# Kernel tuning notes

Measured on AMD Instinct MI355X. Metric: run time of the kernel, lower is better.

Reference implementation:

```python
import jax, jax.numpy as jnp
import numpy as np

B, L, H, NH, F = 32, 200, 256, 4, 2
D = H // NH
C = (2 + F) ** 2  # 16 fused attention streams (queries x keys)
SCALE = np.float32(1.0 / np.sqrt(D))
EPS = 1e-12


def setup_inputs() -> dict:
    key = jax.random.key(0)
    ks = jax.random.split(key, 16)
    p = lambda k, sh: jax.random.normal(k, sh, jnp.float32) * 0.02
    causal = jnp.tril(jnp.ones((L, L), jnp.float32))
    return {
        "input_tensor": jax.random.normal(ks[0], (B, L, H), jnp.float32),
        "attribute_table": jax.random.normal(ks[1], (F, B, L, 1, H), jnp.float32),
        "position_embedding": jax.random.normal(ks[2], (B, L, H), jnp.float32),
        "attention_mask": ((1.0 - causal) * -10000.0)[None, None],  # [1,1,L,L] additive causal mask
        "Wq": p(ks[3], (H, H)), "bq": jnp.zeros((H,), jnp.float32),
        "Wk": p(ks[4], (H, H)), "bk": jnp.zeros((H,), jnp.float32),
        "Wv": p(ks[5], (H, H)), "bv": jnp.zeros((H,), jnp.float32),
        "Wqp": p(ks[6], (H, H)), "bqp": jnp.zeros((H,), jnp.float32),
        "Wkp": p(ks[7], (H, H)), "bkp": jnp.zeros((H,), jnp.float32),
        "Wvp": p(ks[8], (H, H)), "bvp": jnp.zeros((H,), jnp.float32),
        "Wq_a": p(ks[9], (F, H, H)), "bq_a": jnp.zeros((F, H), jnp.float32),
        "Wk_a": p(ks[10], (F, H, H)), "bk_a": jnp.zeros((F, H), jnp.float32),
        "Wv_a": p(ks[11], (F, H, H)), "bv_a": jnp.zeros((F, H), jnp.float32),
        "Wf1": p(ks[12], (L, L)), "bf1": jnp.zeros((L,), jnp.float32),
        "Wf2": p(ks[13], (L, 1)), "bf2": jnp.zeros((1,), jnp.float32),
        "Wd": p(ks[14], (H, H)), "bd": jnp.zeros((H,), jnp.float32),
        "gamma": jnp.ones((H,), jnp.float32),
        "beta": jnp.zeros((H,), jnp.float32),
    }


def _forward(input_tensor, attribute_table, position_embedding, attention_mask,
             Wq, bq, Wk, bk, Wv, bv, Wqp, bqp, Wkp, bkp, Wvp, bvp,
             Wq_a, bq_a, Wk_a, bk_a, Wv_a, bv_a,
             Wf1, bf1, Wf2, bf2, Wd, bd, gamma, beta):
    Bv = input_tensor.shape[0]
    heads = lambda x: x.reshape(Bv, L, NH, D).transpose(0, 2, 1, 3)  # [B,h,L,d]
    q_i = heads(input_tensor @ Wq + bq)
    k_i = heads(input_tensor @ Wk + bk)
    v_i = heads(input_tensor @ Wv + bv)
    q_p = heads(position_embedding @ Wqp + bqp)
    k_p = heads(position_embedding @ Wkp + bkp)
    # NOTE: position values and attribute values are computed by the original module
    # but never consumed (context uses only item values), so we skip them.
    attr = attribute_table[:, :, :, 0, :]  # squeeze(-2) -> [F,B,L,H]
    ah = lambda y: y.reshape(F, Bv, L, NH, D).transpose(0, 1, 3, 2, 4)  # [F,B,h,L,d]
    q_a = ah(jnp.einsum('fblh,fhe->fble', attr, Wq_a) + bq_a[:, None, None, :])
    k_a = ah(jnp.einsum('fblh,fhe->fble', attr, Wk_a) + bk_a[:, None, None, :])
    # query stream order: [item, pos, attr_0..attr_{F-1}]; key order: [item, attr_0..attr_{F-1}, pos]
    Q = jnp.concatenate([q_i[:, None], q_p[:, None], q_a.transpose(1, 0, 2, 3, 4)], axis=1)  # [B,2+F,h,L,d]
    K = jnp.concatenate([k_i[:, None], k_a.transpose(1, 0, 2, 3, 4), k_p[:, None]], axis=1)  # [B,2+F,h,L,d]
    # all query-stream x key-stream raw scores, flattened query-major -> [B,C,h,L,L]
    scores = jnp.einsum('bqhld,bkhmd->bqkhlm', Q, K).reshape(Bv, C, NH, L, L)
    ac = scores.transpose(0, 2, 3, 1, 4)  # [B,h,L,C,L]
    # gate fusion (VanillaAttention over the C stream axis)
    energy = (jax.nn.relu(ac @ Wf1 + bf1) @ Wf2)[..., 0] + bf2  # [B,h,L,C]
    w = jax.nn.softmax(energy, axis=-1)
    attn = jnp.einsum('bhlcm,bhlc->bhlm', ac, w) * SCALE + attention_mask
    probs = jax.nn.softmax(attn, axis=-1)
    ctx = jnp.einsum('bhlm,bhmd->bhld', probs, v_i)
    ctx = ctx.transpose(0, 2, 1, 3).reshape(Bv, L, H)
    x = ctx @ Wd + bd + input_tensor
    mu = x.mean(-1, keepdims=True)
    var = ((x - mu) ** 2).mean(-1, keepdims=True)
    return (x - mu) / jnp.sqrt(var + EPS) * gamma + beta


def reference(input_tensor, attribute_table, position_embedding, attention_mask,
              Wq, bq, Wk, bk, Wv, bv, Wqp, bqp, Wkp, bkp, Wvp, bvp,
              Wq_a, bq_a, Wk_a, bk_a, Wv_a, bv_a,
              Wf1, bf1, Wf2, bf2, Wd, bd, gamma, beta):
    return _forward(input_tensor, attribute_table, position_embedding, attention_mask,
                    Wq, bq, Wk, bk, Wv, bv, Wqp, bqp, Wkp, bkp, Wvp, bvp,
                    Wq_a, bq_a, Wk_a, bk_a, Wv_a, bv_a,
                    Wf1, bf1, Wf2, bf2, Wd, bd, gamma, beta)
```

## Files before the change

### kernel.cpp

```cpp
#include <hip/hip_runtime.h>
#include <hip/hip_bf16.h>

#define B_    32
#define L_    200
#define H_    256
#define NH_   4
#define D_    64
#define SCALE_ 0.125f
#define EPS_  1e-12f

typedef unsigned short u16;
typedef __attribute__((ext_vector_type(8))) short bf16x8;
typedef __attribute__((ext_vector_type(4))) float f32x4;

__device__ __forceinline__ float b2f(u16 u) {
  union { unsigned int i; float f; } v; v.i = ((unsigned int)u) << 16; return v.f;
}
__device__ __forceinline__ u16 f2b(float f) {
  union { float f; unsigned int i; } v; v.f = f;
  unsigned int u = v.i;
  return (u16)((u + 0x7FFF + ((u >> 16) & 1)) >> 16);
}

struct PrepArgs {
  const float* X[4];
  const float* W[10];
  const float* Wf1;
};
struct BiasArgs { const float* Bi[9]; };

__global__ __launch_bounds__(256) void prep_kernel(PrepArgs pa,
    u16* __restrict__ Xb, u16* __restrict__ Wb, u16* __restrict__ Wf1T,
    u16* __restrict__ Qb, u16* __restrict__ Kb) {
  const int N0 = 6553600, N1 = 655360, N2 = 46592, N3 = 786432, N4 = 262144;
  const int total = N0 + N1 + N2 + N3 + N4;
  for (int idx = blockIdx.x * 256 + threadIdx.x; idx < total;
       idx += gridDim.x * 256) {
    if (idx < N0) {
      int i = idx;
      int s = i / 1638400, r = i % 1638400;
      Xb[i] = f2b(pa.X[s][r]);
    } else if (idx < N0 + N1) {
      int i = idx - N0;
      int z = i >> 16, rem = i & 65535, n = rem >> 8, k = rem & 255;
      Wb[i] = f2b(pa.W[z][k * 256 + n]);
    } else if (idx < N0 + N1 + N2) {
      int i = idx - N0 - N1;
      int n = i / 224, m = i % 224;
      Wf1T[i] = (n < 200 && m < 200) ? f2b(pa.Wf1[m * 200 + n]) : (u16)0;
    } else if (idx < N0 + N1 + N2 + N3) {
      int i = idx - N0 - N1 - N2;
      int mat = i / 1536, rr = i % 1536;
      Qb[((size_t)mat * 224 + 200 + rr / 64) * 64 + (rr & 63)] = 0;
    } else {
      int i = idx - N0 - N1 - N2 - N3;
      int mat = i / 512, rr = i % 512;
      Kb[((size_t)mat * 208 + 200 + rr / 64) * 64 + (rr & 63)] = 0;
    }
  }
}

__global__ __launch_bounds__(256) void proj_mfma(
    const u16* __restrict__ Xb, const u16* __restrict__ Wb, BiasArgs ba,
    u16* __restrict__ Qb, u16* __restrict__ Kb, u16* __restrict__ Ktd,
    u16* __restrict__ Vt) {
  const int mb = blockIdx.x, z = blockIdx.y;
  const int row0 = mb * 64;
  const int tid = threadIdx.x;
  const int wv = tid >> 6, ln = tid & 63;
  const int lrow = ln & 15, lk8 = ln >> 4;

  const int zx = (z < 4) ? z : (z == 4 ? 0 : z == 5 ? 2 : z == 6 ? 3 : z == 7 ? 1 : 0);
  const u16* X  = Xb + (size_t)zx * 1638400;
  const u16* Wz = Wb + (size_t)z * 65536;
  const float* bias = ba.Bi[z];

  __shared__ u16 tile[64][264];

  f32x4 c[4][4];
#pragma unroll
  for (int mt = 0; mt < 4; ++mt)
#pragma unroll
    for (int nt = 0; nt < 4; ++nt) c[mt][nt] = (f32x4){0.f, 0.f, 0.f, 0.f};

#pragma unroll
  for (int ks = 0; ks < 8; ++ks) {
    bf16x8 a[4], bfr[4];
#pragma unroll
    for (int mt = 0; mt < 4; ++mt)
      a[mt] = *(const bf16x8*)&X[(size_t)(row0 + mt * 16 + lrow) * 256 + ks * 32 + lk8 * 8];
#pragma unroll
    for (int nt = 0; nt < 4; ++nt)
      bfr[nt] = *(const bf16x8*)&Wz[(size_t)(wv * 64 + nt * 16 + lrow) * 256 + ks * 32 + lk8 * 8];
#pragma unroll
    for (int mt = 0; mt < 4; ++mt)
#pragma unroll
      for (int nt = 0; nt < 4; ++nt)
        c[mt][nt] = __builtin_amdgcn_mfma_f32_16x16x32_bf16(a[mt], bfr[nt], c[mt][nt], 0, 0, 0);
  }

#pragma unroll
  for (int nt = 0; nt < 4; ++nt) {
    int n = wv * 64 + nt * 16 + lrow;
    float bn = bias[n];
#pragma unroll
    for (int mt = 0; mt < 4; ++mt)
#pragma unroll
      for (int j = 0; j < 4; ++j)
        tile[mt * 16 + lk8 * 4 + j][n] = f2b(c[mt][nt][j] + bn);
  }
  __syncthreads();

  if (z < 4) {
    int m = tid >> 2, h = tid & 3;
    int gm = row0 + m, b = gm / 200, l = gm - b * 200;
    u16* dst = &Qb[((size_t)((b * 4 + h) * 4 + z) * 224 + l) * 64];
    const u16* srcp = &tile[m][h * 64];
#pragma unroll
    for (int q = 0; q < 4; ++q)
      *(bf16x8*)&dst[q * 8] = *(const bf16x8*)&srcp[q * 8];
  } else if (z < 8) {
    {
      int m = tid >> 2, h = tid & 3;
      int gm = row0 + m, b = gm / 200, l = gm - b * 200;
      u16* dst = &Kb[((size_t)((b * 4 + h) * 4 + (z - 4)) * 208 + l) * 64];
      const u16* srcp = &tile[m][h * 64];
#pragma unroll
      for (int q = 0; q < 4; ++q)
        *(bf16x8*)&dst[q * 8] = *(const bf16x8*)&srcp[q * 8];
    }
    {
      int h2 = tid >> 6, d = tid & 63;
#pragma unroll
      for (int ch = 0; ch < 8; ++ch) {
        int m0c = ch * 8;
        int gmc = row0 + m0c, bc = gmc / 200, lc = gmc - bc * 200;
        int matc = (bc * 4 + h2) * 4 + (z - 4);
        bf16x8 o;
#pragma unroll
        for (int q = 0; q < 8; ++q) o[q] = (short)tile[m0c + q][h2 * 64 + d];
        *(bf16x8*)&Ktd[((size_t)matc * 64 + d) * 224 + lc] = o;
      }
    }
  } else {
    int h2 = tid >> 6, d = tid & 63;
#pragma unroll
    for (int ch = 0; ch < 8; ++ch) {
      int m0c = ch * 8;
      int gmc = row0 + m0c, bc = gmc / 200, lc = gmc - bc * 200;
      int bhc = bc * 4 + h2;
      bf16x8 o;
#pragma unroll
      for (int q = 0; q < 8; ++q) o[q] = (short)tile[m0c + q][h2 * 64 + d];
      *(bf16x8*)&Vt[((size_t)bhc * 64 + d) * 224 + lc] = o;
    }
  }
}

__global__ __launch_bounds__(256) void kw_mfma(
    const u16* __restrict__ Wf1T, const u16* __restrict__ Ktd,
    u16* __restrict__ KWb) {
  const int mat = blockIdx.x;
  const int tid = threadIdx.x;
  const int wv = tid >> 6, ln = tid & 63;
  const int lrow = ln & 15, lk8 = ln >> 4;
  const u16* Bt = Ktd + (size_t)mat * 64 * 224;

  for (int nt = wv; nt < 13; nt += 4) {
    f32x4 cd0 = {0.f,0.f,0.f,0.f}, cd1 = {0.f,0.f,0.f,0.f};
    f32x4 cd2 = {0.f,0.f,0.f,0.f}, cd3 = {0.f,0.f,0.f,0.f};
#pragma unroll
    for (int ks = 0; ks < 7; ++ks) {
      bf16x8 a = *(const bf16x8*)&Wf1T[(size_t)(nt * 16 + lrow) * 224 + ks * 32 + lk8 * 8];
      bf16x8 b0 = *(const bf16x8*)&Bt[(size_t)(0 * 16 + lrow) * 224 + ks * 32 + lk8 * 8];
      bf16x8 b1 = *(const bf16x8*)&Bt[(size_t)(1 * 16 + lrow) * 224 + ks * 32 + lk8 * 8];
      bf16x8 b2 = *(const bf16x8*)&Bt[(size_t)(2 * 16 + lrow) * 224 + ks * 32 + lk8 * 8];
      bf16x8 b3 = *(const bf16x8*)&Bt[(size_t)(3 * 16 + lrow) * 224 + ks * 32 + lk8 * 8];
      cd0 = __builtin_amdgcn_mfma_f32_16x16x32_bf16(a, b0, cd0, 0, 0, 0);
      cd1 = __builtin_amdgcn_mfma_f32_16x16x32_bf16(a, b1, cd1, 0, 0, 0);
      cd2 = __builtin_amdgcn_mfma_f32_16x16x32_bf16(a, b2, cd2, 0, 0, 0);
      cd3 = __builtin_amdgcn_mfma_f32_16x16x32_bf16(a, b3, cd3, 0, 0, 0);
    }
#pragma unroll
    for (int j = 0; j < 4; ++j) {
      size_t base = ((size_t)mat * 256 + nt * 16 + lk8 * 4 + j) * 64 + lrow;
      KWb[base + 0]  = f2b(cd0[j]);
      KWb[base + 16] = f2b(cd1[j]);
      KWb[base + 32] = f2b(cd2[j]);
      KWb[base + 48] = f2b(cd3[j]);
    }
  }
}

__global__ __launch_bounds__(256) void fused_kernel(
    const u16* __restrict__ Qb, const u16* __restrict__ Kb,
    const u16* __restrict__ KWb, const u16* __restrict__ Vt,
    const float* __restrict__ mask, const float* __restrict__ bf1,
    const float* __restrict__ Wf2, u16* __restrict__ Ctxb) {
  const int bid = blockIdx.x;
  const int wid = (bid & 7) * 112 + (bid >> 3);
  const int lt = wid % 7, bh = wid / 7;
  const int l0 = lt * 32;
  const int b = bh >> 2, h = bh & 3;
  const int tid = threadIdx.x;
  const int wv = tid >> 6, ln = tid & 63;
  const int lrow = ln & 15, lk8 = ln >> 4;

  __shared__ u16  qwpb[8448];
  __shared__ float att[32 * 208];
  __shared__ float El[512];
  __shared__ float wg[512];
  __shared__ float b1s[256], w2s[256];

  b1s[tid] = (tid < 200) ? bf1[tid] : 0.f;
  w2s[tid] = (tid < 200) ? Wf2[tid] : 0.f;
  __syncthreads();

  {
    const u16* KWm = KWb + (size_t)(bh * 4 + wv) * 16384;
#pragma unroll
    for (int mt = 0; mt < 2; ++mt) {
      bf16x8 aE[4][2];
#pragma unroll
      for (int cq = 0; cq < 4; ++cq)
#pragma unroll
        for (int ks = 0; ks < 2; ++ks)
          aE[cq][ks] = *(const bf16x8*)&Qb[((size_t)(bh * 4 + cq) * 224 + l0 + mt * 16 + lrow) * 64 + ks * 32 + lk8 * 8];

      f32x4 eacc[4];
#pragma unroll
      for (int cq = 0; cq < 4; ++cq) eacc[cq] = (f32x4){0.f, 0.f, 0.f, 0.f};

      bf16x8 b0 = *(const bf16x8*)&KWm[lrow * 64 + lk8 * 8];
      bf16x8 b1 = *(const bf16x8*)&KWm[lrow * 64 + 32 + lk8 * 8];
#pragma unroll 1
      for (int nt = 0; nt < 13; ++nt) {
        bf16x8 nb0 = b0, nb1 = b1;
        if (nt < 12) {
          nb0 = *(const bf16x8*)&KWm[((nt + 1) * 16 + lrow) * 64 + lk8 * 8];
          nb1 = *(const bf16x8*)&KWm[((nt + 1) * 16 + lrow) * 64 + 32 + lk8 * 8];
        }
        f32x4 c0 = {0.f, 0.f, 0.f, 0.f}, c1 = {0.f, 0.f, 0.f, 0.f};
        f32x4 c2 = {0.f, 0.f, 0.f, 0.f}, c3 = {0.f, 0.f, 0.f, 0.f};
        c0 = __builtin_amdgcn_mfma_f32_16x16x32_bf16(aE[0][0], b0, c0, 0, 0, 0);
        c1 = __builtin_amdgcn_mfma_f32_16x16x32_bf16(aE[1][0], b0, c1, 0, 0, 0);
        c2 = __builtin_amdgcn_mfma_f32_16x16x32_bf16(aE[2][0], b0, c2, 0, 0, 0);
        c3 = __builtin_amdgcn_mfma_f32_16x16x32_bf16(aE[3][0], b0, c3, 0, 0, 0);
        c0 = __builtin_amdgcn_mfma_f32_16x16x32_bf16(aE[0][1], b1, c0, 0, 0, 0);
        c1 = __builtin_amdgcn_mfma_f32_16x16x32_bf16(aE[1][1], b1, c1, 0, 0, 0);
        c2 = __builtin_amdgcn_mfma_f32_16x16x32_bf16(aE[2][1], b1, c2, 0, 0, 0);
        c3 = __builtin_amdgcn_mfma_f32_16x16x32_bf16(aE[3][1], b1, c3, 0, 0, 0);
        float b1n = b1s[nt * 16 + lrow];
        float w2n = w2s[nt * 16 + lrow];
#pragma unroll
        for (int j = 0; j < 4; ++j) {
          eacc[0][j] += fmaxf(c0[j] + b1n, 0.f) * w2n;
          eacc[1][j] += fmaxf(c1[j] + b1n, 0.f) * w2n;
          eacc[2][j] += fmaxf(c2[j] + b1n, 0.f) * w2n;
          eacc[3][j] += fmaxf(c3[j] + b1n, 0.f) * w2n;
        }
        b0 = nb0; b1 = nb1;
      }

#pragma unroll
      for (int cq = 0; cq < 4; ++cq)
#pragma unroll
        for (int j = 0; j < 4; ++j) {
          float v = eacc[cq][j];
          v += __shfl_xor(v, 1);
          v += __shfl_xor(v, 2);
          v += __shfl_xor(v, 4);
          v += __shfl_xor(v, 8);
          if (lrow == 0)
            El[(mt * 16 + lk8 * 4 + j) * 16 + cq * 4 + wv] = v;
        }
    }
  }
  __syncthreads();

#pragma unroll
  for (int it = 0; it < 2; ++it) {
    int l = it * 16 + (tid >> 4), c = tid & 15;
    float e = El[l * 16 + c];
    float mx = e;
    mx = fmaxf(mx, __shfl_xor(mx, 8));
    mx = fmaxf(mx, __shfl_xor(mx, 4));
    mx = fmaxf(mx, __shfl_xor(mx, 2));
    mx = fmaxf(mx, __shfl_xor(mx, 1));
    float ex = __expf(e - mx);
    float s = ex;
    s += __shfl_xor(s, 8);
    s += __shfl_xor(s, 4);
    s += __shfl_xor(s, 2);
    s += __shfl_xor(s, 1);
    wg[l * 16 + c] = ex / s;
  }
  __syncthreads();

  {
    int lq = tid >> 3, d0 = (tid & 7) * 8;
    float qf[4][8];
#pragma unroll
    for (int cq = 0; cq < 4; ++cq) {
      bf16x8 q8 = *(const bf16x8*)&Qb[((size_t)(bh * 4 + cq) * 224 + l0 + lq) * 64 + d0];
#pragma unroll
      for (int j = 0; j < 8; ++j) qf[cq][j] = b2f((u16)q8[j]);
    }
    float wv_[16];
#pragma unroll
    for (int c = 0; c < 16; ++c) wv_[c] = wg[lq * 16 + c];
#pragma unroll
    for (int ck = 0; ck < 4; ++ck) {
      float a[8];
#pragma unroll
      for (int j = 0; j < 8; ++j)
        a[j] = wv_[0 * 4 + ck] * qf[0][j] + wv_[1 * 4 + ck] * qf[1][j] +
               wv_[2 * 4 + ck] * qf[2][j] + wv_[3 * 4 + ck] * qf[3][j];
#pragma unroll
      for (int p = 0; p < 4; ++p) {
        unsigned int pk = f2b(a[2 * p]) | ((unsigned int)f2b(a[2 * p + 1]) << 16);
        *(unsigned int*)&qwpb[lq * 264 + ck * 64 + d0 + 2 * p] = pk;
      }
    }
  }
  __syncthreads();

  for (int mt = wv; mt < 13; mt += 4) {
    f32x4 sc0 = {0.f, 0.f, 0.f, 0.f}, sc1 = {0.f, 0.f, 0.f, 0.f};
#pragma unroll
    for (int ks = 0; ks < 8; ++ks) {
      int ck = ks >> 1, dd = (ks & 1) * 32 + lk8 * 8;
      const u16* Km = Kb + (size_t)(bh * 4 + ck) * 208 * 64;
      bf16x8 bK = *(const bf16x8*)&Km[(mt * 16 + lrow) * 64 + dd];
      bf16x8 a0 = *(const bf16x8*)&qwpb[lrow * 264 + ck * 64 + dd];
      bf16x8 a1 = *(const bf16x8*)&qwpb[(16 + lrow) * 264 + ck * 64 + dd];
      sc0 = __builtin_amdgcn_mfma_f32_16x16x32_bf16(a0, bK, sc0, 0, 0, 0);
      sc1 = __builtin_amdgcn_mfma_f32_16x16x32_bf16(a1, bK, sc1, 0, 0, 0);
    }
    int m = mt * 16 + lrow;
    int gm = (m > 199) ? 199 : m;
#pragma unroll
    for (int j = 0; j < 4; ++j) {
      int la = lk8 * 4 + j;
      int gla = l0 + la; if (gla > 199) gla = 199;
      int lb = 16 + lk8 * 4 + j;
      int glb = l0 + lb; if (glb > 199) glb = 199;
      att[la * 208 + m] = sc0[j] * SCALE_ + mask[(size_t)gla * 200 + gm];
      att[lb * 208 + m] = sc1[j] * SCALE_ + mask[(size_t)glb * 200 + gm];
    }
  }
  __syncthreads();

  u16* pb = qwpb;
#pragma unroll
  for (int it = 0; it < 2; ++it) {
    int l = it * 16 + (tid >> 4), j = tid & 15;
    float mx = -3.0e38f;
    for (int m = j; m < 200; m += 16) mx = fmaxf(mx, att[l * 208 + m]);
    mx = fmaxf(mx, __shfl_xor(mx, 8));
    mx = fmaxf(mx, __shfl_xor(mx, 4));
    mx = fmaxf(mx, __shfl_xor(mx, 2));
    mx = fmaxf(mx, __shfl_xor(mx, 1));
    float s = 0.f;
    for (int m = j; m < 200; m += 16) {
      float ex = __expf(att[l * 208 + m] - mx);
      att[l * 208 + m] = ex;
      s += ex;
    }
    s += __shfl_xor(s, 8);
    s += __shfl_xor(s, 4);
    s += __shfl_xor(s, 2);
    s += __shfl_xor(s, 1);
    float rinv = 1.f / s;
    for (int m = j; m < 200; m += 16) pb[l * 232 + m] = f2b(att[l * 208 + m] * rinv);
    for (int m = 200 + j; m < 232; m += 16) pb[l * 232 + m] = 0;
  }
  __syncthreads();

  {
    const u16* Vb = Vt + (size_t)bh * 64 * 224;
    f32x4 pc0 = {0.f, 0.f, 0.f, 0.f}, pc1 = {0.f, 0.f, 0.f, 0.f};
#pragma unroll
    for (int ks = 0; ks < 7; ++ks) {
      int mm = ks * 32 + lk8 * 8;
      bf16x8 a0 = *(const bf16x8*)&pb[lrow * 232 + mm];
      bf16x8 a1 = *(const bf16x8*)&pb[(16 + lrow) * 232 + mm];
      bf16x8 bV = *(const bf16x8*)&Vb[(wv * 16 + lrow) * 224 + mm];
      pc0 = __builtin_amdgcn_mfma_f32_16x16x32_bf16(a0, bV, pc0, 0, 0, 0);
      pc1 = __builtin_amdgcn_mfma_f32_16x16x32_bf16(a1, bV, pc1, 0, 0, 0);
    }
#pragma unroll
    for (int j = 0; j < 4; ++j) {
      int la = lk8 * 4 + j, lb = 16 + lk8 * 4 + j;
      int gla = l0 + la, glb = l0 + lb;
      int d = h * 64 + wv * 16 + lrow;
      if (gla < 200) Ctxb[((size_t)b * 200 + gla) * 256 + d] = f2b(pc0[j]);
      if (glb < 200) Ctxb[((size_t)b * 200 + glb) * 256 + d] = f2b(pc1[j]);
    }
  }
}

__global__ __launch_bounds__(256) void out_ln_kernel(
    const u16* __restrict__ Ctxb, const u16* __restrict__ WdT,
    const float* __restrict__ bd, const float* __restrict__ input,
    const float* __restrict__ gamma, const float* __restrict__ beta,
    float* __restrict__ out) {
  const int row0 = blockIdx.x * 32;
  const int tid = threadIdx.x;
  const int wv = tid >> 6, ln = tid & 63;
  const int lrow = ln & 15, lk8 = ln >> 4;

  __shared__ float redA[32][65];
  __shared__ float redB[32][65];
  __shared__ float mus[32], rsd[32];

  f32x4 c[2][4];
#pragma unroll
  for (int mt = 0; mt < 2; ++mt)
#pragma unroll
    for (int nt = 0; nt < 4; ++nt) c[mt][nt] = (f32x4){0.f, 0.f, 0.f, 0.f};

#pragma unroll
  for (int ks = 0; ks < 8; ++ks) {
    bf16x8 a[2], bfr[4];
#pragma unroll
    for (int mt = 0; mt < 2; ++mt)
      a[mt] = *(const bf16x8*)&Ctxb[(size_t)(row0 + mt * 16 + lrow) * 256 + ks * 32 + lk8 * 8];
#pragma unroll
    for (int nt = 0; nt < 4; ++nt)
      bfr[nt] = *(const bf16x8*)&WdT[(size_t)(wv * 64 + nt * 16 + lrow) * 256 + ks * 32 + lk8 * 8];
#pragma unroll
    for (int mt = 0; mt < 2; ++mt)
#pragma unroll
      for (int nt = 0; nt < 4; ++nt)
        c[mt][nt] = __builtin_amdgcn_mfma_f32_16x16x32_bf16(a[mt], bfr[nt], c[mt][nt], 0, 0, 0);
  }

  float s1[2][4], s2[2][4];
#pragma unroll
  for (int mt = 0; mt < 2; ++mt)
#pragma unroll
    for (int j = 0; j < 4; ++j) { s1[mt][j] = 0.f; s2[mt][j] = 0.f; }

#pragma unroll
  for (int nt = 0; nt < 4; ++nt) {
    int n = wv * 64 + nt * 16 + lrow;
    float bdn = bd[n];
#pragma unroll
    for (int mt = 0; mt < 2; ++mt) {
      int mbase = row0 + mt * 16 + lk8 * 4;
#pragma unroll
      for (int j = 0; j < 4; ++j) {
        float x = c[mt][nt][j] + bdn + input[(size_t)(mbase + j) * 256 + n];
        c[mt][nt][j] = x;
        s1[mt][j] += x;
        s2[mt][j] += x * x;
      }
    }
  }
#pragma unroll
  for (int mt = 0; mt < 2; ++mt)
#pragma unroll
    for (int j = 0; j < 4; ++j) {
      redA[mt * 16 + lk8 * 4 + j][wv * 16 + lrow] = s1[mt][j];
      redB[mt * 16 + lk8 * 4 + j][wv * 16 + lrow] = s2[mt][j];
    }
  __syncthreads();
  if (tid < 32) {
    float a = 0.f, b2 = 0.f;
#pragma unroll 8
    for (int i = 0; i < 64; ++i) { a += redA[tid][i]; b2 += redB[tid][i]; }
    float mu = a * (1.f / 256.f);
    float var = b2 * (1.f / 256.f) - mu * mu;
    mus[tid] = mu;
    rsd[tid] = rsqrtf(var + EPS_);
  }
  __syncthreads();
#pragma unroll
  for (int nt = 0; nt < 4; ++nt) {
    int n = wv * 64 + nt * 16 + lrow;
    float g = gamma[n], be = beta[n];
#pragma unroll
    for (int mt = 0; mt < 2; ++mt) {
#pragma unroll
      for (int j = 0; j < 4; ++j) {
        int r = mt * 16 + lk8 * 4 + j;
        out[(size_t)(row0 + r) * 256 + n] = (c[mt][nt][j] - mus[r]) * rsd[r] * g + be;
      }
    }
  }
}

extern "C" void kernel_launch(void* const* d_in, const int* in_sizes, int n_in,
                              void* d_out, int out_size, void* d_ws, size_t ws_size,
                              hipStream_t stream) {
  const float* input = (const float*)d_in[0];
  const float* attrt = (const float*)d_in[1];
  const float* pos   = (const float*)d_in[2];
  const float* mask  = (const float*)d_in[3];
  const float* Wq  = (const float*)d_in[4];   const float* bq  = (const float*)d_in[5];
  const float* Wk  = (const float*)d_in[6];   const float* bk  = (const float*)d_in[7];
  const float* Wv  = (const float*)d_in[8];   const float* bv  = (const float*)d_in[9];
  const float* Wqp = (const float*)d_in[10];  const float* bqp = (const float*)d_in[11];
  const float* Wkp = (const float*)d_in[12];  const float* bkp = (const float*)d_in[13];
  const float* Wq_a = (const float*)d_in[16]; const float* bq_a = (const float*)d_in[17];
  const float* Wk_a = (const float*)d_in[18]; const float* bk_a = (const float*)d_in[19];
  const float* Wf1 = (const float*)d_in[22];  const float* bf1 = (const float*)d_in[23];
  const float* Wf2 = (const float*)d_in[24];
  const float* Wd  = (const float*)d_in[26];  const float* bd  = (const float*)d_in[27];
  const float* gamma = (const float*)d_in[28]; const float* beta = (const float*)d_in[29];

  const float* attr0 = attrt;
  const float* attr1 = attrt + (size_t)B_ * L_ * H_;

  u16* wsu  = (u16*)d_ws;
  u16* Xb   = wsu;
  u16* Wb   = Xb + 6553600;
  u16* Wf1T = Wb + 655360;
  u16* Qb   = Wf1T + 46592;
  u16* Kb   = Qb + 7340032;
  u16* Ktd  = Kb + 6815744;
  u16* Vt   = Ktd + 7340032;
  u16* KWb  = Vt + 1835008;
  u16* Ctxb = KWb + 8388608;

  PrepArgs pp;
  pp.X[0] = input; pp.X[1] = pos; pp.X[2] = attr0; pp.X[3] = attr1;
  pp.W[0] = Wq;  pp.W[1] = Wqp; pp.W[2] = Wq_a; pp.W[3] = Wq_a + 65536;
  pp.W[4] = Wk;  pp.W[5] = Wk_a; pp.W[6] = Wk_a + 65536; pp.W[7] = Wkp;
  pp.W[8] = Wv;  pp.W[9] = Wd;
  pp.Wf1 = Wf1;

  BiasArgs ba;
  ba.Bi[0] = bq;  ba.Bi[1] = bqp;  ba.Bi[2] = bq_a; ba.Bi[3] = bq_a + 256;
  ba.Bi[4] = bk;  ba.Bi[5] = bk_a; ba.Bi[6] = bk_a + 256; ba.Bi[7] = bkp;
  ba.Bi[8] = bv;

  prep_kernel<<<dim3(4096), dim3(256), 0, stream>>>(pp, Xb, Wb, Wf1T, Qb, Kb);
  proj_mfma<<<dim3(100, 9), dim3(256), 0, stream>>>(Xb, Wb, ba, Qb, Kb, Ktd, Vt);
  kw_mfma<<<dim3(512), dim3(256), 0, stream>>>(Wf1T, Ktd, KWb);
  fused_kernel<<<dim3(896), dim3(256), 0, stream>>>(Qb, Kb, KWb, Vt,
                                                    mask, bf1, Wf2, Ctxb);
  out_ln_kernel<<<dim3(200), dim3(256), 0, stream>>>(Ctxb, Wb + 9 * 65536, bd,
                                                     input, gamma, beta,
                                                     (float*)d_out);
}
```

Baseline: 156.2 us.

## Keep attention scores in registers and fuse softmax with cross-wave reductions

```diff
diff --git a/kernel.cpp b/kernel.cpp
--- a/kernel.cpp
+++ b/kernel.cpp
@@ -207,10 +207,11 @@
   const int lrow = ln & 15, lk8 = ln >> 4;
 
   __shared__ u16  qwpb[8448];
-  __shared__ float att[32 * 208];
   __shared__ float El[512];
   __shared__ float wg[512];
   __shared__ float b1s[256], w2s[256];
+  __shared__ float redm[32][4];
+  __shared__ float reds[32][4];
 
   b1s[tid] = (tid < 200) ? bf1[tid] : 0.f;
   w2s[tid] = (tid < 200) ? Wf2[tid] : 0.f;
@@ -325,55 +326,127 @@
   }
   __syncthreads();
 
-  for (int mt = wv; mt < 13; mt += 4) {
-    f32x4 sc0 = {0.f, 0.f, 0.f, 0.f}, sc1 = {0.f, 0.f, 0.f, 0.f};
-#pragma unroll
-    for (int ks = 0; ks < 8; ++ks) {
-      int ck = ks >> 1, dd = (ks & 1) * 32 + lk8 * 8;
-      const u16* Km = Kb + (size_t)(bh * 4 + ck) * 208 * 64;
-      bf16x8 bK = *(const bf16x8*)&Km[(mt * 16 + lrow) * 64 + dd];
-      bf16x8 a0 = *(const bf16x8*)&qwpb[lrow * 264 + ck * 64 + dd];
-      bf16x8 a1 = *(const bf16x8*)&qwpb[(16 + lrow) * 264 + ck * 64 + dd];
-      sc0 = __builtin_amdgcn_mfma_f32_16x16x32_bf16(a0, bK, sc0, 0, 0, 0);
-      sc1 = __builtin_amdgcn_mfma_f32_16x16x32_bf16(a1, bK, sc1, 0, 0, 0);
-    }
-    int m = mt * 16 + lrow;
-    int gm = (m > 199) ? 199 : m;
-#pragma unroll
-    for (int j = 0; j < 4; ++j) {
-      int la = lk8 * 4 + j;
-      int gla = l0 + la; if (gla > 199) gla = 199;
-      int lb = 16 + lk8 * 4 + j;
-      int glb = l0 + lb; if (glb > 199) glb = 199;
-      att[la * 208 + m] = sc0[j] * SCALE_ + mask[(size_t)gla * 200 + gm];
-      att[lb * 208 + m] = sc1[j] * SCALE_ + mask[(size_t)glb * 200 + gm];
-    }
-  }
-  __syncthreads();
+  f32x4 s0r[4], s1r[4];
+#pragma unroll
+  for (int q = 0; q < 4; ++q) {
+    s0r[q] = (f32x4){0.f, 0.f, 0.f, 0.f};
+    s1r[q] = (f32x4){0.f, 0.f, 0.f, 0.f};
+  }
+#pragma unroll
+  for (int q = 0; q < 4; ++q) {
+    const int mt = wv + q * 4;
+    if (mt < 13) {
+      f32x4 sc0 = {0.f, 0.f, 0.f, 0.f}, sc1 = {0.f, 0.f, 0.f, 0.f};
+#pragma unroll
+      for (int ks = 0; ks < 8; ++ks) {
+        int ck = ks >> 1, dd = (ks & 1) * 32 + lk8 * 8;
+        const u16* Km = Kb + (size_t)(bh * 4 + ck) * 208 * 64;
+        bf16x8 bK = *(const bf16x8*)&Km[(mt * 16 + lrow) * 64 + dd];
+        bf16x8 a0 = *(const bf16x8*)&qwpb[lrow * 264 + ck * 64 + dd];
+        bf16x8 a1 = *(const bf16x8*)&qwpb[(16 + lrow) * 264 + ck * 64 + dd];
+        sc0 = __builtin_amdgcn_mfma_f32_16x16x32_bf16(a0, bK, sc0, 0, 0, 0);
+        sc1 = __builtin_amdgcn_mfma_f32_16x16x32_bf16(a1, bK, sc1, 0, 0, 0);
+      }
+      s0r[q] = sc0; s1r[q] = sc1;
+    }
+  }
+
+  float e0[4][4], e1[4][4];
+#pragma unroll
+  for (int q = 0; q < 4; ++q) {
+    const int mt = wv + q * 4;
+    const int m = mt * 16 + lrow;
+#pragma unroll
+    for (int j = 0; j < 4; ++j) {
+      if (mt < 13 && m < 200) {
+        int gla = l0 + lk8 * 4 + j;      if (gla > 199) gla = 199;
+        int glb = l0 + 16 + lk8 * 4 + j; if (glb > 199) glb = 199;
+        e0[q][j] = s0r[q][j] * SCALE_ + mask[(size_t)gla * 200 + m];
+        e1[q][j] = s1r[q][j] * SCALE_ + mask[(size_t)glb * 200 + m];
+      } else {
+        e0[q][j] = -3.0e38f;
+        e1[q][j] = -3.0e38f;
+      }
+    }
+  }
+  float M0[4], M1[4];
+#pragma unroll
+  for (int j = 0; j < 4; ++j) {
+    M0[j] = fmaxf(fmaxf(e0[0][j], e0[1][j]), fmaxf(e0[2][j], e0[3][j]));
+    M1[j] = fmaxf(fmaxf(e1[0][j], e1[1][j]), fmaxf(e1[2][j], e1[3][j]));
+  }
+#pragma unroll
+  for (int o = 8; o >= 1; o >>= 1)
+#pragma unroll
+    for (int j = 0; j < 4; ++j) {
+      M0[j] = fmaxf(M0[j], __shfl_xor(M0[j], o));
+      M1[j] = fmaxf(M1[j], __shfl_xor(M1[j], o));
+    }
+  if (lrow == 0) {
+#pragma unroll
+    for (int j = 0; j < 4; ++j) {
+      redm[lk8 * 4 + j][wv] = M0[j];
+      redm[16 + lk8 * 4 + j][wv] = M1[j];
+    }
+  }
+  __syncthreads();
+#pragma unroll
+  for (int j = 0; j < 4; ++j) {
+    int la = lk8 * 4 + j;
+    M0[j] = fmaxf(fmaxf(redm[la][0], redm[la][1]), fmaxf(redm[la][2], redm[la][3]));
+    M1[j] = fmaxf(fmaxf(redm[16 + la][0], redm[16 + la][1]),
+                  fmaxf(redm[16 + la][2], redm[16 + la][3]));
+  }
+  float S0[4] = {0.f, 0.f, 0.f, 0.f}, S1[4] = {0.f, 0.f, 0.f, 0.f};
+#pragma unroll
+  for (int q = 0; q < 4; ++q)
+#pragma unroll
+    for (int j = 0; j < 4; ++j) {
+      e0[q][j] = __expf(e0[q][j] - M0[j]);
+      e1[q][j] = __expf(e1[q][j] - M1[j]);
+      S0[j] += e0[q][j];
+      S1[j] += e1[q][j];
+    }
+#pragma unroll
+  for (int o = 8; o >= 1; o >>= 1)
+#pragma unroll
+    for (int j = 0; j < 4; ++j) {
+      S0[j] += __shfl_xor(S0[j], o);
+      S1[j] += __shfl_xor(S1[j], o);
+    }
+  if (lrow == 0) {
+#pragma unroll
+    for (int j = 0; j < 4; ++j) {
+      reds[lk8 * 4 + j][wv] = S0[j];
+      reds[16 + lk8 * 4 + j][wv] = S1[j];
+    }
+  }
+  __syncthreads();
+  float R0[4], R1[4];
+#pragma unroll
+  for (int j = 0; j < 4; ++j) {
+    int la = lk8 * 4 + j;
+    R0[j] = 1.f / (reds[la][0] + reds[la][1] + reds[la][2] + reds[la][3]);
+    R1[j] = 1.f / (reds[16 + la][0] + reds[16 + la][1] +
+                   reds[16 + la][2] + reds[16 + la][3]);
+  }
 
   u16* pb = qwpb;
-#pragma unroll
-  for (int it = 0; it < 2; ++it) {
-    int l = it * 16 + (tid >> 4), j = tid & 15;
-    float mx = -3.0e38f;
-    for (int m = j; m < 200; m += 16) mx = fmaxf(mx, att[l * 208 + m]);
-    mx = fmaxf(mx, __shfl_xor(mx, 8));
-    mx = fmaxf(mx, __shfl_xor(mx, 4));
-    mx = fmaxf(mx, __shfl_xor(mx, 2));
-    mx = fmaxf(mx, __shfl_xor(mx, 1));
-    float s = 0.f;
-    for (int m = j; m < 200; m += 16) {
-      float ex = __expf(att[l * 208 + m] - mx);
-      att[l * 208 + m] = ex;
-      s += ex;
-    }
-    s += __shfl_xor(s, 8);
-    s += __shfl_xor(s, 4);
-    s += __shfl_xor(s, 2);
-    s += __shfl_xor(s, 1);
-    float rinv = 1.f / s;
-    for (int m = j; m < 200; m += 16) pb[l * 232 + m] = f2b(att[l * 208 + m] * rinv);
-    for (int m = 200 + j; m < 232; m += 16) pb[l * 232 + m] = 0;
+  for (int idx = tid; idx < 768; idx += 256) {
+    int l = idx / 24, mm = idx % 24;
+    pb[l * 232 + 208 + mm] = 0;
+  }
+#pragma unroll
+  for (int q = 0; q < 4; ++q) {
+    const int mt = wv + q * 4;
+    if (mt < 13) {
+      const int m = mt * 16 + lrow;
+#pragma unroll
+      for (int j = 0; j < 4; ++j) {
+        pb[(lk8 * 4 + j) * 232 + m] = f2b(e0[q][j] * R0[j]);
+        pb[(16 + lk8 * 4 + j) * 232 + m] = f2b(e1[q][j] * R1[j]);
+      }
+    }
   }
   __syncthreads();
 
```

Result: faster. 138.9 us (median of 2 runs) (-11.1%).
